# Performance work log

Hardware: AMD Instinct MI355X
Metric: run time of the kernel (lower is better)

The kernel has to match this reference:

```python
import jax, jax.numpy as jnp
import numpy as np

N_NODES = 100_000
N_EDGES = 800_000
D = 96
BN_EPS = 1e-5
LEAKY_SLOPE = 0.01


def setup_inputs() -> dict:
    key = jax.random.key(0)
    ks = jax.random.split(key, 9)
    x = jax.random.normal(ks[0], (N_NODES, D), dtype=jnp.float32)
    edge_index = jax.random.randint(ks[1], (2, N_EDGES), 0, N_NODES, dtype=jnp.int64)
    s = 0.05
    return {
        "x": x,
        "edge_index": edge_index,
        # SAGEConv #1 (mean aggregator, bias=False)
        "W_self1": jax.random.normal(ks[2], (D, D), dtype=jnp.float32) * s,
        "W_neigh1": jax.random.normal(ks[3], (D, D), dtype=jnp.float32) * s,
        # SAGEConv #2 (pool aggregator): fc_pool has bias, fc_self/fc_neigh bias=False
        "W_pool": jax.random.normal(ks[4], (D, D), dtype=jnp.float32) * s,
        "b_pool": jax.random.normal(ks[5], (D,), dtype=jnp.float32) * s,
        "W_self2": jax.random.normal(ks[6], (D, D), dtype=jnp.float32) * s,
        "W_neigh2": jax.random.normal(ks[7], (D, D), dtype=jnp.float32) * s,
        # BatchNorm affine params
        "g1": jnp.ones((D,), jnp.float32),
        "beta1": jnp.zeros((D,), jnp.float32),
        "g2": jnp.ones((D,), jnp.float32),
        "beta2": jnp.zeros((D,), jnp.float32),
    }


def _batch_norm(h, gamma, beta):
    # training-mode BatchNorm1d: biased batch stats over nodes
    mu = h.mean(axis=0)
    var = jnp.mean(jnp.square(h - mu), axis=0)
    return gamma * (h - mu) * jax.lax.rsqrt(var + BN_EPS) + beta


def _forward(x, edge_index, W_self1, W_neigh1, W_pool, b_pool, W_self2, W_neigh2,
             g1, beta1, g2, beta2):
    src, dst = edge_index[0], edge_index[1]
    n = x.shape[0]
    deg = jax.ops.segment_sum(jnp.ones((src.shape[0],), x.dtype), dst, num_segments=n)

    # ---- SAGEConv (mean): h_neigh = mean_{u in N(v)} x_u ; out = x W_self + h_neigh W_neigh
    agg_sum = jax.ops.segment_sum(x[src], dst, num_segments=n)          # [N, D]
    h_mean = agg_sum / jnp.maximum(deg, 1.0)[:, None]                   # 0 for isolated nodes
    out1 = x @ W_self1 + h_mean @ W_neigh1
    out1 = _batch_norm(out1, g1, beta1)

    # ---- SAGEConv (pool): h_neigh = max_{u in N(v)} relu(x_u W_pool + b_pool)
    hp = jax.nn.relu(x @ W_pool + b_pool)                               # [N, D]
    agg_max = jax.ops.segment_max(hp[src], dst, num_segments=n)        # -inf where empty
    h_max = jnp.where(deg[:, None] > 0, agg_max, 0.0)
    out2 = x @ W_self2 + h_max @ W_neigh2
    out2 = _batch_norm(out2, g2, beta2)

    return jax.nn.leaky_relu(out1 + out2, negative_slope=LEAKY_SLOPE)


def reference(x, edge_index, W_self1, W_neigh1, W_pool, b_pool, W_self2, W_neigh2,
              g1, beta1, g2, beta2):
    return _forward(x, edge_index, W_self1, W_neigh1, W_pool, b_pool,
                    W_self2, W_neigh2, g1, beta1, g2, beta2)
```

## Files before the change

kernel.cpp:

```cpp
#include <hip/hip_runtime.h>

#define NN 100000
#define NE 800000
#define DD 96
#define NROWPAD 100096
#define GBLK 782
#define SCAN_BLOCKS 100
#define SCAN_CHUNK 1000

typedef __attribute__((ext_vector_type(8))) short bf16x8;
typedef __attribute__((ext_vector_type(4))) float f32x4;
typedef unsigned short u16;
typedef unsigned int u32;

#define MFMA16 __builtin_amdgcn_mfma_f32_16x16x32_bf16

#define OFF_DEG      0u
#define OFF_ROWSTART 100000u
#define OFF_CURSOR   200004u
#define OFF_BSUM     300004u
#define OFF_STATS    300132u
#define OFF_PARAMS   300516u
#define OFF_WT       300900u
#define OFF_CSR      323940u
#define ROWF         4804608u
#define OFF_XBF      1123940u
#define OFF_HMBF     (OFF_XBF + ROWF)
#define OFF_HXBF     (OFF_HMBF + ROWF)
#define OFF_HPBF     (OFF_HXBF + ROWF)

__device__ __forceinline__ u16 f2b(float f) {
  u32 u = __float_as_uint(f);
  u += 0x7FFFu + ((u >> 16) & 1u);
  return (u16)(u >> 16);
}
__device__ __forceinline__ float b2f(short h) {
  return __uint_as_float(((u32)(u16)h) << 16);
}

__global__ void wprep_kernel(const float* __restrict__ Ws1, const float* __restrict__ Wn1,
                             const float* __restrict__ Ws2, const float* __restrict__ Wn2,
                             const float* __restrict__ Wp, u16* __restrict__ wt) {
  int idx = blockIdx.x * 256 + threadIdx.x;
  if (idx >= 5 * 9216) return;
  int m = idx / 9216, r = idx % 9216;
  int k = r / 96, c = r % 96;
  const float* W = (m == 0) ? Ws1 : (m == 1) ? Wn1 : (m == 2) ? Ws2 : (m == 3) ? Wn2 : Wp;
  wt[m * 9216 + c * 96 + k] = f2b(W[k * 96 + c]);
}

__global__ void cvt_kernel(const float* __restrict__ x, u16* __restrict__ xbf) {
  int i = blockIdx.x * 256 + threadIdx.x;
  if (i >= NN * 12) return;
  float4 a = reinterpret_cast<const float4*>(x)[i * 2];
  float4 b = reinterpret_cast<const float4*>(x)[i * 2 + 1];
  bf16x8 v;
  v[0] = (short)f2b(a.x); v[1] = (short)f2b(a.y); v[2] = (short)f2b(a.z); v[3] = (short)f2b(a.w);
  v[4] = (short)f2b(b.x); v[5] = (short)f2b(b.y); v[6] = (short)f2b(b.z); v[7] = (short)f2b(b.w);
  reinterpret_cast<bf16x8*>(xbf)[i] = v;
}

__global__ void deg_kernel(const int* __restrict__ dst, int* __restrict__ deg) {
  int e = blockIdx.x * blockDim.x + threadIdx.x;
  if (e >= NE) return;
  atomicAdd(&deg[dst[e]], 1);
}

__global__ void scan_sum_kernel(const int* __restrict__ deg, int* __restrict__ bsum) {
  __shared__ int red[256];
  int t = threadIdx.x;
  int base = blockIdx.x * SCAN_CHUNK;
  int s = 0;
  for (int i = t; i < SCAN_CHUNK; i += 256) s += deg[base + i];
  red[t] = s;
  __syncthreads();
  for (int off = 128; off > 0; off >>= 1) {
    if (t < off) red[t] += red[t + off];
    __syncthreads();
  }
  if (t == 0) bsum[blockIdx.x] = red[0];
}

__global__ void scan_bsum_kernel(int* __restrict__ bsum, int* __restrict__ row_start) {
  __shared__ int sm[128];
  int t = threadIdx.x;
  int v = (t < SCAN_BLOCKS) ? bsum[t] : 0;
  sm[t] = v;
  __syncthreads();
  for (int off = 1; off < 128; off <<= 1) {
    int u = 0;
    if (t >= off) u = sm[t - off];
    __syncthreads();
    if (t >= off) sm[t] += u;
    __syncthreads();
  }
  if (t < SCAN_BLOCKS) bsum[t] = sm[t] - v;
  if (t == SCAN_BLOCKS - 1) row_start[NN] = sm[t];
}

__global__ void scan_final_kernel(const int* __restrict__ deg,
                                  const int* __restrict__ bsum,
                                  int* __restrict__ row_start,
                                  int* __restrict__ cursor) {
  __shared__ int sm[256];
  int t = threadIdx.x;
  int base = blockIdx.x * SCAN_CHUNK + t * 4;
  int4 d = {0, 0, 0, 0};
  if (t < 250) d = *reinterpret_cast<const int4*>(deg + base);
  int tot = d.x + d.y + d.z + d.w;
  sm[t] = tot;
  __syncthreads();
  for (int off = 1; off < 256; off <<= 1) {
    int u = 0;
    if (t >= off) u = sm[t - off];
    __syncthreads();
    if (t >= off) sm[t] += u;
    __syncthreads();
  }
  if (t < 250) {
    int run = bsum[blockIdx.x] + sm[t] - tot;
    int4 rs;
    rs.x = run;
    rs.y = run + d.x;
    rs.z = run + d.x + d.y;
    rs.w = run + d.x + d.y + d.z;
    *reinterpret_cast<int4*>(row_start + base) = rs;
    *reinterpret_cast<int4*>(cursor + base) = rs;
  }
}

__global__ void fill_csr_kernel(const int* __restrict__ src,
                                const int* __restrict__ dst,
                                int* __restrict__ cursor,
                                int* __restrict__ csr) {
  int e = blockIdx.x * blockDim.x + threadIdx.x;
  if (e >= NE) return;
  int pos = atomicAdd(&cursor[dst[e]], 1);
  csr[pos] = src[e];
}

__global__ __launch_bounds__(512) void hp_gemm_kernel(const u16* __restrict__ xbf,
                                                      const u16* __restrict__ wt,
                                                      const float* __restrict__ bp,
                                                      u16* __restrict__ hpbf) {
  __shared__ bf16x8 wl[1152];
  int t = threadIdx.x;
  const bf16x8* wg = reinterpret_cast<const bf16x8*>(wt + 4 * 9216);
  for (int j = t; j < 1152; j += 512) wl[j] = wg[j];
  __syncthreads();
  int w = t >> 6, lane = t & 63;
  int i = lane & 15, g = lane >> 4;
  int row_base = blockIdx.x * 128 + w * 16;
  size_t arow = (size_t)(row_base + i) * 12;
  bf16x8 ax[3];
#pragma unroll
  for (int kb = 0; kb < 3; ++kb) ax[kb] = reinterpret_cast<const bf16x8*>(xbf)[arow + kb * 4 + g];
  for (int nt = 0; nt < 6; ++nt) {
    f32x4 acc = {0.f, 0.f, 0.f, 0.f};
    int bch = (nt * 16 + i) * 12;
#pragma unroll
    for (int kb = 0; kb < 3; ++kb)
      acc = MFMA16(ax[kb], wl[bch + kb * 4 + g], acc, 0, 0, 0);
    int col = nt * 16 + i;
    float bias = bp[col];
#pragma unroll
    for (int r = 0; r < 4; ++r) {
      int grow = row_base + g * 4 + r;
      if (grow < NN)
        hpbf[(size_t)grow * 96 + col] = f2b(fmaxf(acc[r] + bias, 0.0f));
    }
  }
}

__global__ __launch_bounds__(256) void gather_kernel(const u16* __restrict__ xbf,
                                                     const u16* __restrict__ hpbf,
                                                     const int* __restrict__ row_start,
                                                     const int* __restrict__ csr,
                                                     u16* __restrict__ hmbf,
                                                     u16* __restrict__ hxbf) {
  int t = threadIdx.x;
  int node = blockIdx.x * 64 + (t >> 2);
  if (node >= NN) return;
  int ln = t & 3;
  int beg = row_start[node], end = row_start[node + 1];
  float s[3][8], mx[3][8];
#pragma unroll
  for (int c = 0; c < 3; ++c)
#pragma unroll
    for (int e8 = 0; e8 < 8; ++e8) { s[c][e8] = 0.f; mx[c][e8] = 0.f; }
  for (int e = beg; e < end; ++e) {
    int srow = csr[e];
    size_t base = (size_t)srow * 12;
#pragma unroll
    for (int c = 0; c < 3; ++c) {
      bf16x8 xv = reinterpret_cast<const bf16x8*>(xbf)[base + ln + c * 4];
      bf16x8 hv = reinterpret_cast<const bf16x8*>(hpbf)[base + ln + c * 4];
#pragma unroll
      for (int e8 = 0; e8 < 8; ++e8) {
        s[c][e8] += b2f(xv[e8]);
        mx[c][e8] = fmaxf(mx[c][e8], b2f(hv[e8]));
      }
    }
  }
  float inv = (end > beg) ? 1.0f / (float)(end - beg) : 0.0f;
  size_t obase = (size_t)node * 12;
#pragma unroll
  for (int c = 0; c < 3; ++c) {
    bf16x8 vm, vx;
#pragma unroll
    for (int e8 = 0; e8 < 8; ++e8) {
      vm[e8] = (short)f2b(s[c][e8] * inv);
      vx[e8] = (short)f2b(mx[c][e8]);
    }
    reinterpret_cast<bf16x8*>(hmbf)[obase + ln + c * 4] = vm;
    reinterpret_cast<bf16x8*>(hxbf)[obase + ln + c * 4] = vx;
  }
}

__global__ __launch_bounds__(512) void dualgemm_kernel(const u16* __restrict__ xbf,
                                                       const u16* __restrict__ hmbf,
                                                       const u16* __restrict__ hxbf,
                                                       const u16* __restrict__ wt,
                                                       float* __restrict__ stats,
                                                       const float* __restrict__ params,
                                                       float* __restrict__ out,
                                                       int mode) {
  __shared__ bf16x8 wl[4608];
  __shared__ float smst[384];
  int t = threadIdx.x;
  const bf16x8* wg = reinterpret_cast<const bf16x8*>(wt);
  for (int j = t; j < 4608; j += 512) wl[j] = wg[j];
  if (mode == 0)
    for (int j = t; j < 384; j += 512) smst[j] = 0.f;
  __syncthreads();
  int w = t >> 6, lane = t & 63;
  int i = lane & 15, g = lane >> 4;
  int row_base = blockIdx.x * 128 + w * 16;
  size_t arow = (size_t)(row_base + i) * 12;
  bf16x8 ax[3], am[3], ah[3];
#pragma unroll
  for (int kb = 0; kb < 3; ++kb) {
    ax[kb] = reinterpret_cast<const bf16x8*>(xbf)[arow + kb * 4 + g];
    am[kb] = reinterpret_cast<const bf16x8*>(hmbf)[arow + kb * 4 + g];
    ah[kb] = reinterpret_cast<const bf16x8*>(hxbf)[arow + kb * 4 + g];
  }
  for (int nt = 0; nt < 6; ++nt) {
    f32x4 a1 = {0.f, 0.f, 0.f, 0.f}, a2 = {0.f, 0.f, 0.f, 0.f};
    int bch = (nt * 16 + i) * 12;
#pragma unroll
    for (int kb = 0; kb < 3; ++kb) {
      int bc = bch + kb * 4 + g;
      a1 = MFMA16(ax[kb], wl[bc], a1, 0, 0, 0);
      a1 = MFMA16(am[kb], wl[1152 + bc], a1, 0, 0, 0);
      a2 = MFMA16(ax[kb], wl[2304 + bc], a2, 0, 0, 0);
      a2 = MFMA16(ah[kb], wl[3456 + bc], a2, 0, 0, 0);
    }
    int col = nt * 16 + i;
    if (mode == 0) {
      float s1 = 0, q1 = 0, s2 = 0, q2 = 0;
#pragma unroll
      for (int r = 0; r < 4; ++r) {
        int grow = row_base + g * 4 + r;
        if (grow < NN) {
          float v = a1[r], u = a2[r];
          s1 += v; q1 += v * v; s2 += u; q2 += u * u;
        }
      }
      s1 += __shfl_xor(s1, 16); q1 += __shfl_xor(q1, 16);
      s2 += __shfl_xor(s2, 16); q2 += __shfl_xor(q2, 16);
      s1 += __shfl_xor(s1, 32); q1 += __shfl_xor(q1, 32);
      s2 += __shfl_xor(s2, 32); q2 += __shfl_xor(q2, 32);
      if (g == 0) {
        atomicAdd(&smst[col], s1);
        atomicAdd(&smst[96 + col], q1);
        atomicAdd(&smst[192 + col], s2);
        atomicAdd(&smst[288 + col], q2);
      }
    } else {
      float p1 = params[col], c1 = params[96 + col];
      float p2 = params[192 + col], c2 = params[288 + col];
#pragma unroll
      for (int r = 0; r < 4; ++r) {
        int grow = row_base + g * 4 + r;
        if (grow < NN) {
          float v = p1 * a1[r] + c1 + p2 * a2[r] + c2;
          v = v > 0.f ? v : 0.01f * v;
          out[(size_t)grow * 96 + col] = v;
        }
      }
    }
  }
  if (mode == 0) {
    __syncthreads();
    for (int j = t; j < 384; j += 512) atomicAdd(&stats[j], smst[j]);
  }
}

__global__ void finalize_kernel(const float* __restrict__ stats,
                                const float* __restrict__ g1, const float* __restrict__ beta1,
                                const float* __restrict__ g2, const float* __restrict__ beta2,
                                float* __restrict__ params) {
  int c = threadIdx.x;
  if (c >= 96) return;
  const float inv_n = 1.0f / NN;
  float mu1 = stats[c] * inv_n;
  float var1 = fmaxf(stats[96 + c] * inv_n - mu1 * mu1, 0.0f);
  float is1 = rsqrtf(var1 + 1e-5f);
  float a1 = g1[c] * is1;
  params[c] = a1;
  params[96 + c] = beta1[c] - a1 * mu1;
  float mu2 = stats[192 + c] * inv_n;
  float var2 = fmaxf(stats[288 + c] * inv_n - mu2 * mu2, 0.0f);
  float is2 = rsqrtf(var2 + 1e-5f);
  float a2 = g2[c] * is2;
  params[192 + c] = a2;
  params[288 + c] = beta2[c] - a2 * mu2;
}

extern "C" void kernel_launch(void* const* d_in, const int* in_sizes, int n_in,
                              void* d_out, int out_size, void* d_ws, size_t ws_size,
                              hipStream_t stream) {
  const float* x       = (const float*)d_in[0];
  const int*   ei      = (const int*)d_in[1];
  const float* W_self1 = (const float*)d_in[2];
  const float* W_neigh1= (const float*)d_in[3];
  const float* W_pool  = (const float*)d_in[4];
  const float* b_pool  = (const float*)d_in[5];
  const float* W_self2 = (const float*)d_in[6];
  const float* W_neigh2= (const float*)d_in[7];
  const float* g1      = (const float*)d_in[8];
  const float* beta1   = (const float*)d_in[9];
  const float* g2      = (const float*)d_in[10];
  const float* beta2   = (const float*)d_in[11];
  float* out = (float*)d_out;

  float* ws = (float*)d_ws;
  int*   deg       = (int*)(ws + OFF_DEG);
  int*   row_start = (int*)(ws + OFF_ROWSTART);
  int*   cursor    = (int*)(ws + OFF_CURSOR);
  int*   bsum      = (int*)(ws + OFF_BSUM);
  float* stats     = ws + OFF_STATS;
  float* params    = ws + OFF_PARAMS;
  u16*   wt        = (u16*)(ws + OFF_WT);
  int*   csr       = (int*)(ws + OFF_CSR);
  u16*   xbf       = (u16*)(ws + OFF_XBF);
  u16*   hmbf      = (u16*)(ws + OFF_HMBF);
  u16*   hxbf      = (u16*)(ws + OFF_HXBF);
  u16*   hpbf      = (u16*)(ws + OFF_HPBF);

  const int* src = ei;
  const int* dst = ei + NE;

  hipMemsetAsync(deg, 0, NN * sizeof(int), stream);
  hipMemsetAsync(stats, 0, 384 * sizeof(float), stream);

  wprep_kernel<<<(5 * 9216 + 255) / 256, 256, 0, stream>>>(W_self1, W_neigh1, W_self2,
                                                           W_neigh2, W_pool, wt);
  cvt_kernel<<<(NN * 12 + 255) / 256, 256, 0, stream>>>(x, xbf);

  deg_kernel<<<(NE + 255) / 256, 256, 0, stream>>>(dst, deg);
  scan_sum_kernel<<<SCAN_BLOCKS, 256, 0, stream>>>(deg, bsum);
  scan_bsum_kernel<<<1, 128, 0, stream>>>(bsum, row_start);
  scan_final_kernel<<<SCAN_BLOCKS, 256, 0, stream>>>(deg, bsum, row_start, cursor);
  fill_csr_kernel<<<(NE + 255) / 256, 256, 0, stream>>>(src, dst, cursor, csr);

  hp_gemm_kernel<<<GBLK, 512, 0, stream>>>(xbf, wt, b_pool, hpbf);

  gather_kernel<<<(NN + 63) / 64, 256, 0, stream>>>(xbf, hpbf, row_start, csr, hmbf, hxbf);

  dualgemm_kernel<<<GBLK, 512, 0, stream>>>(xbf, hmbf, hxbf, wt, stats, params, out, 0);
  finalize_kernel<<<1, 128, 0, stream>>>(stats, g1, beta1, g2, beta2, params);
  dualgemm_kernel<<<GBLK, 512, 0, stream>>>(xbf, hmbf, hxbf, wt, stats, params, out, 1);
}
```

Before: 288.0 us.

## Fuse x conversion into pool GEMM and interleave x/hp rows for gather

```diff
diff --git a/kernel.cpp b/kernel.cpp
--- a/kernel.cpp
+++ b/kernel.cpp
@@ -23,11 +23,9 @@
 #define OFF_PARAMS   300516u
 #define OFF_WT       300900u
 #define OFF_CSR      323940u
-#define ROWF         4804608u
-#define OFF_XBF      1123940u
-#define OFF_HMBF     (OFF_XBF + ROWF)
-#define OFF_HXBF     (OFF_HMBF + ROWF)
-#define OFF_HPBF     (OFF_HXBF + ROWF)
+#define OFF_XH       1123940u
+#define OFF_HMBF     10733156u
+#define OFF_HXBF     15537764u
 
 __device__ __forceinline__ u16 f2b(float f) {
   u32 u = __float_as_uint(f);
@@ -49,17 +47,6 @@
   wt[m * 9216 + c * 96 + k] = f2b(W[k * 96 + c]);
 }
 
-__global__ void cvt_kernel(const float* __restrict__ x, u16* __restrict__ xbf) {
-  int i = blockIdx.x * 256 + threadIdx.x;
-  if (i >= NN * 12) return;
-  float4 a = reinterpret_cast<const float4*>(x)[i * 2];
-  float4 b = reinterpret_cast<const float4*>(x)[i * 2 + 1];
-  bf16x8 v;
-  v[0] = (short)f2b(a.x); v[1] = (short)f2b(a.y); v[2] = (short)f2b(a.z); v[3] = (short)f2b(a.w);
-  v[4] = (short)f2b(b.x); v[5] = (short)f2b(b.y); v[6] = (short)f2b(b.z); v[7] = (short)f2b(b.w);
-  reinterpret_cast<bf16x8*>(xbf)[i] = v;
-}
-
 __global__ void deg_kernel(const int* __restrict__ dst, int* __restrict__ deg) {
   int e = blockIdx.x * blockDim.x + threadIdx.x;
   if (e >= NE) return;
@@ -139,10 +126,10 @@
   csr[pos] = src[e];
 }
 
-__global__ __launch_bounds__(512) void hp_gemm_kernel(const u16* __restrict__ xbf,
+__global__ __launch_bounds__(512) void hp_gemm_kernel(const float* __restrict__ x,
                                                       const u16* __restrict__ wt,
                                                       const float* __restrict__ bp,
-                                                      u16* __restrict__ hpbf) {
+                                                      u16* __restrict__ xh) {
   __shared__ bf16x8 wl[1152];
   int t = threadIdx.x;
   const bf16x8* wg = reinterpret_cast<const bf16x8*>(wt + 4 * 9216);
@@ -151,10 +138,21 @@
   int w = t >> 6, lane = t & 63;
   int i = lane & 15, g = lane >> 4;
   int row_base = blockIdx.x * 128 + w * 16;
-  size_t arow = (size_t)(row_base + i) * 12;
+  int grow_a = row_base + i;
+  int lrow = grow_a < NN ? grow_a : NN - 1;
+  const float4* xr = reinterpret_cast<const float4*>(x + (size_t)lrow * 96);
+  bf16x8* xhv = reinterpret_cast<bf16x8*>(xh);
   bf16x8 ax[3];
 #pragma unroll
-  for (int kb = 0; kb < 3; ++kb) ax[kb] = reinterpret_cast<const bf16x8*>(xbf)[arow + kb * 4 + g];
+  for (int kb = 0; kb < 3; ++kb) {
+    float4 p = xr[(kb * 4 + g) * 2];
+    float4 q = xr[(kb * 4 + g) * 2 + 1];
+    bf16x8 v;
+    v[0] = (short)f2b(p.x); v[1] = (short)f2b(p.y); v[2] = (short)f2b(p.z); v[3] = (short)f2b(p.w);
+    v[4] = (short)f2b(q.x); v[5] = (short)f2b(q.y); v[6] = (short)f2b(q.z); v[7] = (short)f2b(q.w);
+    ax[kb] = v;
+    xhv[(size_t)grow_a * 24 + kb * 4 + g] = v;
+  }
   for (int nt = 0; nt < 6; ++nt) {
     f32x4 acc = {0.f, 0.f, 0.f, 0.f};
     int bch = (nt * 16 + i) * 12;
@@ -166,58 +164,84 @@
 #pragma unroll
     for (int r = 0; r < 4; ++r) {
       int grow = row_base + g * 4 + r;
-      if (grow < NN)
-        hpbf[(size_t)grow * 96 + col] = f2b(fmaxf(acc[r] + bias, 0.0f));
-    }
-  }
-}
-
-__global__ __launch_bounds__(256) void gather_kernel(const u16* __restrict__ xbf,
-                                                     const u16* __restrict__ hpbf,
+      xh[(size_t)grow * 192 + 96 + col] = f2b(fmaxf(acc[r] + bias, 0.0f));
+    }
+  }
+}
+
+__global__ __launch_bounds__(256) void gather_kernel(const u16* __restrict__ xh,
                                                      const int* __restrict__ row_start,
                                                      const int* __restrict__ csr,
                                                      u16* __restrict__ hmbf,
                                                      u16* __restrict__ hxbf) {
   int t = threadIdx.x;
-  int node = blockIdx.x * 64 + (t >> 2);
+  int node = blockIdx.x * 32 + (t & 31);
+  int slot = t >> 5;
+  bool isMax = slot >= 4;
   if (node >= NN) return;
-  int ln = t & 3;
   int beg = row_start[node], end = row_start[node + 1];
-  float s[3][8], mx[3][8];
-#pragma unroll
-  for (int c = 0; c < 3; ++c)
-#pragma unroll
-    for (int e8 = 0; e8 < 8; ++e8) { s[c][e8] = 0.f; mx[c][e8] = 0.f; }
-  for (int e = beg; e < end; ++e) {
-    int srow = csr[e];
-    size_t base = (size_t)srow * 12;
-#pragma unroll
-    for (int c = 0; c < 3; ++c) {
-      bf16x8 xv = reinterpret_cast<const bf16x8*>(xbf)[base + ln + c * 4];
-      bf16x8 hv = reinterpret_cast<const bf16x8*>(hpbf)[base + ln + c * 4];
-#pragma unroll
-      for (int e8 = 0; e8 < 8; ++e8) {
-        s[c][e8] += b2f(xv[e8]);
-        mx[c][e8] = fmaxf(mx[c][e8], b2f(hv[e8]));
-      }
-    }
-  }
-  float inv = (end > beg) ? 1.0f / (float)(end - beg) : 0.0f;
-  size_t obase = (size_t)node * 12;
-#pragma unroll
-  for (int c = 0; c < 3; ++c) {
-    bf16x8 vm, vx;
-#pragma unroll
-    for (int e8 = 0; e8 < 8; ++e8) {
-      vm[e8] = (short)f2b(s[c][e8] * inv);
-      vx[e8] = (short)f2b(mx[c][e8]);
-    }
-    reinterpret_cast<bf16x8*>(hmbf)[obase + ln + c * 4] = vm;
-    reinterpret_cast<bf16x8*>(hxbf)[obase + ln + c * 4] = vx;
-  }
-}
-
-__global__ __launch_bounds__(512) void dualgemm_kernel(const u16* __restrict__ xbf,
+  int cbase = slot * 3;
+  const bf16x8* XH = reinterpret_cast<const bf16x8*>(xh);
+  float acc0[8], acc1[8], acc2[8];
+#pragma unroll
+  for (int j = 0; j < 8; ++j) { acc0[j] = 0.f; acc1[j] = 0.f; acc2[j] = 0.f; }
+  int e = beg;
+  for (; e + 2 <= end; e += 2) {
+    size_t b0 = (size_t)csr[e] * 24 + cbase;
+    size_t b1 = (size_t)csr[e + 1] * 24 + cbase;
+    bf16x8 a0 = XH[b0], a1 = XH[b0 + 1], a2 = XH[b0 + 2];
+    bf16x8 c0 = XH[b1], c1 = XH[b1 + 1], c2 = XH[b1 + 2];
+    if (isMax) {
+#pragma unroll
+      for (int j = 0; j < 8; ++j) {
+        acc0[j] = fmaxf(acc0[j], fmaxf(b2f(a0[j]), b2f(c0[j])));
+        acc1[j] = fmaxf(acc1[j], fmaxf(b2f(a1[j]), b2f(c1[j])));
+        acc2[j] = fmaxf(acc2[j], fmaxf(b2f(a2[j]), b2f(c2[j])));
+      }
+    } else {
+#pragma unroll
+      for (int j = 0; j < 8; ++j) {
+        acc0[j] += b2f(a0[j]) + b2f(c0[j]);
+        acc1[j] += b2f(a1[j]) + b2f(c1[j]);
+        acc2[j] += b2f(a2[j]) + b2f(c2[j]);
+      }
+    }
+  }
+  if (e < end) {
+    size_t b0 = (size_t)csr[e] * 24 + cbase;
+    bf16x8 a0 = XH[b0], a1 = XH[b0 + 1], a2 = XH[b0 + 2];
+    if (isMax) {
+#pragma unroll
+      for (int j = 0; j < 8; ++j) {
+        acc0[j] = fmaxf(acc0[j], b2f(a0[j]));
+        acc1[j] = fmaxf(acc1[j], b2f(a1[j]));
+        acc2[j] = fmaxf(acc2[j], b2f(a2[j]));
+      }
+    } else {
+#pragma unroll
+      for (int j = 0; j < 8; ++j) {
+        acc0[j] += b2f(a0[j]);
+        acc1[j] += b2f(a1[j]);
+        acc2[j] += b2f(a2[j]);
+      }
+    }
+  }
+  float scl = isMax ? 1.0f : ((end > beg) ? 1.0f / (float)(end - beg) : 0.0f);
+  bf16x8 v0, v1, v2;
+#pragma unroll
+  for (int j = 0; j < 8; ++j) {
+    v0[j] = (short)f2b(acc0[j] * scl);
+    v1[j] = (short)f2b(acc1[j] * scl);
+    v2[j] = (short)f2b(acc2[j] * scl);
+  }
+  u16* dstp = isMax ? hxbf : hmbf;
+  int ccol = isMax ? (slot - 4) * 3 : slot * 3;
+  size_t ob = (size_t)node * 12 + ccol;
+  bf16x8* dv = reinterpret_cast<bf16x8*>(dstp);
+  dv[ob] = v0; dv[ob + 1] = v1; dv[ob + 2] = v2;
+}
+
+__global__ __launch_bounds__(512) void dualgemm_kernel(const u16* __restrict__ xh,
                                                        const u16* __restrict__ hmbf,
                                                        const u16* __restrict__ hxbf,
                                                        const u16* __restrict__ wt,
@@ -236,13 +260,14 @@
   int w = t >> 6, lane = t & 63;
   int i = lane & 15, g = lane >> 4;
   int row_base = blockIdx.x * 128 + w * 16;
-  size_t arow = (size_t)(row_base + i) * 12;
+  size_t arowx = (size_t)(row_base + i) * 24;
+  size_t arowh = (size_t)(row_base + i) * 12;
   bf16x8 ax[3], am[3], ah[3];
 #pragma unroll
   for (int kb = 0; kb < 3; ++kb) {
-    ax[kb] = reinterpret_cast<const bf16x8*>(xbf)[arow + kb * 4 + g];
-    am[kb] = reinterpret_cast<const bf16x8*>(hmbf)[arow + kb * 4 + g];
-    ah[kb] = reinterpret_cast<const bf16x8*>(hxbf)[arow + kb * 4 + g];
+    ax[kb] = reinterpret_cast<const bf16x8*>(xh)[arowx + kb * 4 + g];
+    am[kb] = reinterpret_cast<const bf16x8*>(hmbf)[arowh + kb * 4 + g];
+    ah[kb] = reinterpret_cast<const bf16x8*>(hxbf)[arowh + kb * 4 + g];
   }
   for (int nt = 0; nt < 6; ++nt) {
     f32x4 a1 = {0.f, 0.f, 0.f, 0.f}, a2 = {0.f, 0.f, 0.f, 0.f};
@@ -343,10 +368,9 @@
   float* params    = ws + OFF_PARAMS;
   u16*   wt        = (u16*)(ws + OFF_WT);
   int*   csr       = (int*)(ws + OFF_CSR);
-  u16*   xbf       = (u16*)(ws + OFF_XBF);
+  u16*   xh        = (u16*)(ws + OFF_XH);
   u16*   hmbf      = (u16*)(ws + OFF_HMBF);
   u16*   hxbf      = (u16*)(ws + OFF_HXBF);
-  u16*   hpbf      = (u16*)(ws + OFF_HPBF);
 
   const int* src = ei;
   const int* dst = ei + NE;
@@ -356,7 +380,6 @@
 
   wprep_kernel<<<(5 * 9216 + 255) / 256, 256, 0, stream>>>(W_self1, W_neigh1, W_self2,
                                                            W_neigh2, W_pool, wt);
-  cvt_kernel<<<(NN * 12 + 255) / 256, 256, 0, stream>>>(x, xbf);
 
   deg_kernel<<<(NE + 255) / 256, 256, 0, stream>>>(dst, deg);
   scan_sum_kernel<<<SCAN_BLOCKS, 256, 0, stream>>>(deg, bsum);
@@ -364,11 +387,11 @@
   scan_final_kernel<<<SCAN_BLOCKS, 256, 0, stream>>>(deg, bsum, row_start, cursor);
   fill_csr_kernel<<<(NE + 255) / 256, 256, 0, stream>>>(src, dst, cursor, csr);
 
-  hp_gemm_kernel<<<GBLK, 512, 0, stream>>>(xbf, wt, b_pool, hpbf);
-
-  gather_kernel<<<(NN + 63) / 64, 256, 0, stream>>>(xbf, hpbf, row_start, csr, hmbf, hxbf);
-
-  dualgemm_kernel<<<GBLK, 512, 0, stream>>>(xbf, hmbf, hxbf, wt, stats, params, out, 0);
+  hp_gemm_kernel<<<GBLK, 512, 0, stream>>>(x, wt, b_pool, xh);
+
+  gather_kernel<<<(NN + 31) / 32, 256, 0, stream>>>(xh, row_start, csr, hmbf, hxbf);
+
+  dualgemm_kernel<<<GBLK, 512, 0, stream>>>(xh, hmbf, hxbf, wt, stats, params, out, 0);
   finalize_kernel<<<1, 128, 0, stream>>>(stats, g1, beta1, g2, beta2, params);
-  dualgemm_kernel<<<GBLK, 512, 0, stream>>>(xbf, hmbf, hxbf, wt, stats, params, out, 1);
-}
+  dualgemm_kernel<<<GBLK, 512, 0, stream>>>(xh, hmbf, hxbf, wt, stats, params, out, 1);
+}
```

Measured after the change: 278.0 us. 3.5% less time.
